# Optimization experiments

Measured on AMD Instinct MI355X. Metric: run time of the kernel, lower is better.

The kernel has to match this reference:

```python
import jax, jax.numpy as jnp
import numpy as np

NUM_HEADS = 16

def setup_inputs() -> dict:
    key = jax.random.key(0)
    ks = jax.random.split(key, 5)
    b, c, w, h = 2, 1024, 48, 48
    sc = 0.02
    return {
        "x": jax.random.normal(ks[0], (b, c, w, h), jnp.float32),
        "Wqkv": jax.random.normal(ks[1], (3 * c, c), jnp.float32) * sc,
        "bqkv": jax.random.normal(ks[2], (3 * c,), jnp.float32) * sc,
        "Wo": jax.random.normal(ks[3], (c, c), jnp.float32) * sc,
        "bo": jax.random.normal(ks[4], (c,), jnp.float32) * sc,
    }

def reference(x, Wqkv, bqkv, Wo, bo):
    b, c, w, h = x.shape
    n = NUM_HEADS
    hd = c // n
    s = w * h
    # [b,c,w,h] -> tokens [b, s, c]
    xs = x.transpose(0, 2, 3, 1).reshape(b, s, c)
    qkv = xs @ Wqkv.T + bqkv                       # [b, s, 3c]
    # rearrange 'b s (three n hd) -> three b n s hd'
    qkv = qkv.reshape(b, s, 3, n, hd).transpose(2, 0, 3, 1, 4)
    q, k, v = qkv[0], qkv[1], qkv[2]               # [b, n, s, hd]
    score = jnp.einsum('bnqh,bnkh->bnqk', q, k) / jnp.sqrt(jnp.float32(hd))
    # module uses a soft causal mask: subtract 10000 above the diagonal
    mask = 10000.0 * jnp.triu(jnp.ones((s, s), dtype=score.dtype), k=1)
    attn = jax.nn.softmax(score - mask, axis=-1)   # [b, n, s, s]
    z = jnp.einsum('bnqk,bnkh->bqnh', attn, v).reshape(b, s, c)
    out = z @ Wo.T + bo                            # [b, s, c]
    return out.reshape(b, w, h, c).transpose(0, 3, 1, 2)
```

## Files before the change

kernel.cpp:

```cpp
#include <hip/hip_runtime.h>

typedef __bf16 bf16;
typedef __bf16 bf16x8 __attribute__((ext_vector_type(8)));
typedef float floatx4 __attribute__((ext_vector_type(4)));

static constexpr int S = 2304;
static constexpr int C = 1024;
static constexpr int NHEAD = 16;
static constexpr int HDIM = 64;
static constexpr int BATCH = 2;

__global__ __launch_bounds__(256) void k_convert(const float* __restrict__ src,
                                                 bf16* __restrict__ dst, int n8) {
  int i = blockIdx.x * 256 + threadIdx.x;
  if (i >= n8) return;
  float4 a = *(const float4*)(src + (size_t)i * 8);
  float4 b = *(const float4*)(src + (size_t)i * 8 + 4);
  bf16x8 o;
  o[0] = (bf16)a.x; o[1] = (bf16)a.y; o[2] = (bf16)a.z; o[3] = (bf16)a.w;
  o[4] = (bf16)b.x; o[5] = (bf16)b.y; o[6] = (bf16)b.z; o[7] = (bf16)b.w;
  *(bf16x8*)(dst + (size_t)i * 8) = o;
}

__global__ __launch_bounds__(256) void k_transpose(const float* __restrict__ x,
                                                   bf16* __restrict__ xs) {
  __shared__ bf16 T[64 * 72];
  int c0 = blockIdx.x * 64, t0 = blockIdx.y * 64, b = blockIdx.z;
  int tid = threadIdx.x;
  const float* xb = x + (size_t)b * C * S;
#pragma unroll
  for (int it = 0; it < 4; ++it) {
    int idx = it * 256 + tid;
    int rc = idx >> 4, t4 = idx & 15;
    float4 v = *(const float4*)(xb + (size_t)(c0 + rc) * S + t0 + t4 * 4);
    T[(t4 * 4 + 0) * 72 + rc] = (bf16)v.x;
    T[(t4 * 4 + 1) * 72 + rc] = (bf16)v.y;
    T[(t4 * 4 + 2) * 72 + rc] = (bf16)v.z;
    T[(t4 * 4 + 3) * 72 + rc] = (bf16)v.w;
  }
  __syncthreads();
  bf16* xsb = xs + (size_t)b * S * C;
#pragma unroll
  for (int it = 0; it < 2; ++it) {
    int idx = it * 256 + tid;
    int rt = idx >> 3, c8 = idx & 7;
    bf16x8 v;
#pragma unroll
    for (int i = 0; i < 8; ++i) v[i] = T[rt * 72 + c8 * 8 + i];
    *(bf16x8*)(xsb + (size_t)(t0 + rt) * C + c0 + c8 * 8) = v;
  }
}

__device__ __forceinline__ void g2l16(const bf16* g, bf16* l) {
  __builtin_amdgcn_global_load_lds(
      (const __attribute__((address_space(1))) void*)g,
      (__attribute__((address_space(3))) void*)l, 16, 0, 0);
}

template <int EPI>
__global__ __launch_bounds__(256) void k_gemm_bt(const bf16* __restrict__ A,
                                                 const bf16* __restrict__ Bt,
                                                 const float* __restrict__ bias,
                                                 bf16* __restrict__ q,
                                                 bf16* __restrict__ k,
                                                 bf16* __restrict__ v,
                                                 float* __restrict__ outf) {
  constexpr int K = C;
  __shared__ bf16 As[128 * 32];
  __shared__ bf16 Bs[128 * 32];
  int tid = threadIdx.x;
  int w = tid >> 6, lane = tid & 63, ln = lane & 15, quad = lane >> 4;
  int m0 = blockIdx.y * 128, n0 = blockIdx.x * 128;
  int moff = (w >> 1) * 64, noff = (w & 1) * 64;
  floatx4 acc[4][4] = {};

  for (int k0 = 0; k0 < K; k0 += 32) {
    __syncthreads();
#pragma unroll
    for (int it = 0; it < 2; ++it) {
      int cb = (it * 4 + w) * 64;
      int g = cb + lane;
      int row = g >> 2, c4 = g & 3;
      g2l16(A + (size_t)(m0 + row) * K + k0 + c4 * 8, As + cb * 8);
      g2l16(Bt + (size_t)(n0 + row) * K + k0 + c4 * 8, Bs + cb * 8);
    }
    __syncthreads();
    bf16x8 af[4], bfr[4];
#pragma unroll
    for (int i = 0; i < 4; ++i) {
      af[i]  = *(const bf16x8*)(As + (moff + i * 16 + ln) * 32 + quad * 8);
      bfr[i] = *(const bf16x8*)(Bs + (noff + i * 16 + ln) * 32 + quad * 8);
    }
#pragma unroll
    for (int im = 0; im < 4; ++im)
#pragma unroll
      for (int in = 0; in < 4; ++in)
        acc[im][in] = __builtin_amdgcn_mfma_f32_16x16x32_bf16(
            af[im], bfr[in], acc[im][in], 0, 0, 0);
  }

  int bidx = (m0 >= S) ? 1 : 0;
  if (EPI == 0) {
#pragma unroll
    for (int in = 0; in < 4; ++in) {
      int j = n0 + noff + in * 16 + ln;
      float bv = bias[j];
      int three = j >> 10;
      int head = (j >> 6) & 15;
      int hdi = j & 63;
#pragma unroll
      for (int im = 0; im < 4; ++im) {
        int mbase = m0 + moff + im * 16 + quad * 4;
        int tb = mbase - bidx * S;
        if (three == 2) {
          union { ushort4 u; bf16 h[4]; } P;
#pragma unroll
          for (int r = 0; r < 4; ++r) P.h[r] = (bf16)(acc[im][in][r] + bv);
          *(ushort4*)(v + ((size_t)(bidx * NHEAD + head) * HDIM + hdi) * S + tb) = P.u;
        } else {
          bf16* dst = (three == 0 ? q : k) +
                      ((size_t)(bidx * NHEAD + head) * S + tb) * HDIM + hdi;
#pragma unroll
          for (int r = 0; r < 4; ++r) dst[(size_t)r * HDIM] = (bf16)(acc[im][in][r] + bv);
        }
      }
    }
  } else {
#pragma unroll
    for (int in = 0; in < 4; ++in) {
      int co = n0 + noff + in * 16 + ln;
      float bv = bias[co];
#pragma unroll
      for (int im = 0; im < 4; ++im) {
        int mbase = m0 + moff + im * 16 + quad * 4;
        int tb = mbase - bidx * S;
        float4 st;
        st.x = acc[im][in][0] + bv;
        st.y = acc[im][in][1] + bv;
        st.z = acc[im][in][2] + bv;
        st.w = acc[im][in][3] + bv;
        *(float4*)(outf + ((size_t)bidx * C + co) * S + tb) = st;
      }
    }
  }
}

__global__ __launch_bounds__(256) void k_attn(const bf16* __restrict__ Qg,
                                              const bf16* __restrict__ Kg,
                                              const bf16* __restrict__ Vtg,
                                              bf16* __restrict__ z) {
  __shared__ bf16 Ks[64 * 64];
  __shared__ bf16 Vs[64 * 64];
  __shared__ bf16 Pt[64 * 72];
  int p = blockIdx.x, h = blockIdx.y, b = blockIdx.z;
  int bh = b * NHEAD + h;
  int tid = threadIdx.x;
  int w = tid >> 6, lane = tid & 63, ln = lane & 15, quad = lane >> 4;

  const bf16* kb = Kg + (size_t)bh * S * HDIM;
  const bf16* vb = Vtg + (size_t)bh * HDIM * S;

#pragma unroll 1
  for (int half = 0; half < 2; ++half) {
    int qi = half == 0 ? p : 35 - p;
    int q0 = qi * 64;
    int qg = q0 + w * 16 + ln;

    const bf16* qb = Qg + ((size_t)bh * S + qg) * HDIM + quad * 8;
    bf16x8 qf0 = *(const bf16x8*)qb;
    bf16x8 qf1 = *(const bf16x8*)(qb + 32);

    float lsum = 0.f;
    floatx4 o_acc[4] = {};

    for (int kt = 0; kt <= qi; ++kt) {
      __syncthreads();
#pragma unroll
      for (int it = 0; it < 2; ++it) {
        int chunk = it * 256 + tid;
        int row = chunk >> 3, c8 = chunk & 7;
        int cs = c8 ^ (row & 7);
        g2l16(kb + (size_t)(kt * 64 + row) * HDIM + cs * 8, Ks + chunk * 8);
        g2l16(vb + (size_t)row * S + kt * 64 + cs * 8, Vs + chunk * 8);
      }
      __syncthreads();

      floatx4 s_acc[4] = {};
#pragma unroll
      for (int kf = 0; kf < 4; ++kf) {
        int row = kf * 16 + ln;
        int sw = row & 7;
        bf16x8 k0 = *(const bf16x8*)(Ks + row * 64 + ((0 ^ sw) ^ quad) * 8);
        s_acc[kf] = __builtin_amdgcn_mfma_f32_16x16x32_bf16(k0, qf0, s_acc[kf], 0, 0, 0);
        bf16x8 k1 = *(const bf16x8*)(Ks + row * 64 + ((4 ^ sw) ^ quad) * 8);
        s_acc[kf] = __builtin_amdgcn_mfma_f32_16x16x32_bf16(k1, qf1, s_acc[kf], 0, 0, 0);
      }

#pragma unroll
      for (int kf = 0; kf < 4; ++kf) {
        union { ushort4 u; bf16 hh[4]; } P;
#pragma unroll
        for (int r = 0; r < 4; ++r) {
          int kg = kt * 64 + kf * 16 + quad * 4 + r;
          float pv = (kg > qg) ? 0.f : exp2f(s_acc[kf][r] * 0.180336880f);
          lsum += pv;
          P.hh[r] = (bf16)pv;
        }
        *(ushort4*)(Pt + (w * 16 + ln) * 72 + kf * 16 + quad * 4) = P.u;
      }

#pragma unroll
      for (int t = 0; t < 2; ++t) {
        bf16x8 pf = *(const bf16x8*)(Pt + (w * 16 + ln) * 72 + t * 32 + quad * 8);
#pragma unroll
        for (int hf = 0; hf < 4; ++hf) {
          int row = hf * 16 + ln;
          int sw = row & 7;
          bf16x8 vf = *(const bf16x8*)(Vs + row * 64 + (((t * 4 + quad) ^ sw)) * 8);
          o_acc[hf] = __builtin_amdgcn_mfma_f32_16x16x32_bf16(vf, pf, o_acc[hf], 0, 0, 0);
        }
      }
    }

    lsum += __shfl_xor(lsum, 16);
    lsum += __shfl_xor(lsum, 32);
    float inv = 1.f / lsum;

    bf16* dst = z + ((size_t)b * S + qg) * C + h * HDIM + quad * 4;
#pragma unroll
    for (int hf = 0; hf < 4; ++hf) {
      union { ushort4 u; bf16 hh[4]; } P;
#pragma unroll
      for (int r = 0; r < 4; ++r) P.hh[r] = (bf16)(o_acc[hf][r] * inv);
      *(ushort4*)(dst + hf * 16) = P.u;
    }
    __syncthreads();
  }
}

extern "C" void kernel_launch(void* const* d_in, const int* in_sizes, int n_in,
                              void* d_out, int out_size, void* d_ws, size_t ws_size,
                              hipStream_t stream) {
  const float* x    = (const float*)d_in[0];
  const float* Wqkv = (const float*)d_in[1];
  const float* bqkv = (const float*)d_in[2];
  const float* Wo   = (const float*)d_in[3];
  const float* bo   = (const float*)d_in[4];
  float* out = (float*)d_out;

  bf16* ws = (bf16*)d_ws;
  const size_t tok = (size_t)BATCH * S * C;
  bf16* xs   = ws;
  bf16* Qg   = ws + tok;
  bf16* Kg   = ws + 2 * tok;
  bf16* Vtg  = ws + 3 * tok;
  bf16* Wqb  = ws + 4 * tok;
  bf16* Wob  = Wqb + (size_t)3 * C * C;
  bf16* z    = xs;

  k_convert<<<(3 * C * C / 8 + 255) / 256, 256, 0, stream>>>(Wqkv, Wqb, 3 * C * C / 8);
  k_convert<<<(C * C / 8 + 255) / 256, 256, 0, stream>>>(Wo, Wob, C * C / 8);
  k_transpose<<<dim3(C / 64, S / 64, BATCH), 256, 0, stream>>>(x, xs);
  k_gemm_bt<0><<<dim3(3 * C / 128, BATCH * S / 128), 256, 0, stream>>>(
      xs, Wqb, bqkv, Qg, Kg, Vtg, nullptr);
  k_attn<<<dim3(18, NHEAD, BATCH), 256, 0, stream>>>(Qg, Kg, Vtg, z);
  k_gemm_bt<1><<<dim3(C / 128, BATCH * S / 128), 256, 0, stream>>>(
      z, Wob, bo, nullptr, nullptr, nullptr, out);
}
```

Before: 240.8 us.

## Double-buffer K/V tiles and remap attention grid for XCD locality

The attention kernel now double-buffers its K/V LDS tiles. It issues the global-to-LDS loads for the next key tile before computing on the current one, so each iteration needs one barrier instead of two. The paired-half causal load balancing is replaced by a flat 1152-block grid. Block indices map so that each head stays on one XCD (bh = xcd + 8*grp) for L2 reuse of K/V, and the longest query tiles are dispatched first. This doubles the K/V LDS footprint, which may reduce occupancy, and it relies on the hardware scheduler rather than explicit pairing to balance the causal work.

```diff
diff --git a/kernel.cpp b/kernel.cpp
--- a/kernel.cpp
+++ b/kernel.cpp
@@ -149,92 +149,105 @@
                                               const bf16* __restrict__ Kg,
                                               const bf16* __restrict__ Vtg,
                                               bf16* __restrict__ z) {
-  __shared__ bf16 Ks[64 * 64];
-  __shared__ bf16 Vs[64 * 64];
+  __shared__ bf16 Ks[2][64 * 64];
+  __shared__ bf16 Vs[2][64 * 64];
   __shared__ bf16 Pt[64 * 72];
-  int p = blockIdx.x, h = blockIdx.y, b = blockIdx.z;
-  int bh = b * NHEAD + h;
+  int i = blockIdx.x;
+  int xcd = i & 7, j = i >> 3;
+  int grp = j / 36, jq = j % 36;
+  int qi = 35 - jq;
+  int bh = xcd + 8 * grp;
+  int b = bh >> 4, h = bh & 15;
   int tid = threadIdx.x;
   int w = tid >> 6, lane = tid & 63, ln = lane & 15, quad = lane >> 4;
+  int q0 = qi * 64;
+  int qg = q0 + w * 16 + ln;
 
   const bf16* kb = Kg + (size_t)bh * S * HDIM;
   const bf16* vb = Vtg + (size_t)bh * HDIM * S;
 
+  int s_row = tid >> 3, s_c8 = tid & 7;
+  int s_cs = s_c8 ^ (s_row & 7);
+  int s_row2 = (256 + tid) >> 3;
+  int s_cs2 = s_c8 ^ (s_row2 & 7);
+
+  const bf16* qb = Qg + ((size_t)bh * S + qg) * HDIM + quad * 8;
+  bf16x8 qf0 = *(const bf16x8*)qb;
+  bf16x8 qf1 = *(const bf16x8*)(qb + 32);
+
+  float lsum = 0.f;
+  floatx4 o_acc[4] = {};
+
+  {
+    g2l16(kb + (size_t)s_row * HDIM + s_cs * 8, Ks[0] + tid * 8);
+    g2l16(vb + (size_t)s_row * S + s_cs * 8, Vs[0] + tid * 8);
+    g2l16(kb + (size_t)s_row2 * HDIM + s_cs2 * 8, Ks[0] + (256 + tid) * 8);
+    g2l16(vb + (size_t)s_row2 * S + s_cs2 * 8, Vs[0] + (256 + tid) * 8);
+  }
+
 #pragma unroll 1
-  for (int half = 0; half < 2; ++half) {
-    int qi = half == 0 ? p : 35 - p;
-    int q0 = qi * 64;
-    int qg = q0 + w * 16 + ln;
-
-    const bf16* qb = Qg + ((size_t)bh * S + qg) * HDIM + quad * 8;
-    bf16x8 qf0 = *(const bf16x8*)qb;
-    bf16x8 qf1 = *(const bf16x8*)(qb + 32);
-
-    float lsum = 0.f;
-    floatx4 o_acc[4] = {};
-
-    for (int kt = 0; kt <= qi; ++kt) {
-      __syncthreads();
-#pragma unroll
-      for (int it = 0; it < 2; ++it) {
-        int chunk = it * 256 + tid;
-        int row = chunk >> 3, c8 = chunk & 7;
-        int cs = c8 ^ (row & 7);
-        g2l16(kb + (size_t)(kt * 64 + row) * HDIM + cs * 8, Ks + chunk * 8);
-        g2l16(vb + (size_t)row * S + kt * 64 + cs * 8, Vs + chunk * 8);
-      }
-      __syncthreads();
-
-      floatx4 s_acc[4] = {};
-#pragma unroll
-      for (int kf = 0; kf < 4; ++kf) {
-        int row = kf * 16 + ln;
+  for (int kt = 0; kt <= qi; ++kt) {
+    int cur = kt & 1;
+    __syncthreads();
+
+    if (kt < qi) {
+      int nxt = 1 - cur;
+      const bf16* kbn = kb + (size_t)(kt + 1) * 64 * HDIM;
+      const bf16* vbn = vb + (size_t)(kt + 1) * 64;
+      g2l16(kbn + (size_t)s_row * HDIM + s_cs * 8, Ks[nxt] + tid * 8);
+      g2l16(vbn + (size_t)s_row * S + s_cs * 8, Vs[nxt] + tid * 8);
+      g2l16(kbn + (size_t)s_row2 * HDIM + s_cs2 * 8, Ks[nxt] + (256 + tid) * 8);
+      g2l16(vbn + (size_t)s_row2 * S + s_cs2 * 8, Vs[nxt] + (256 + tid) * 8);
+    }
+
+    floatx4 s_acc[4] = {};
+#pragma unroll
+    for (int kf = 0; kf < 4; ++kf) {
+      int row = kf * 16 + ln;
+      int sw = row & 7;
+      bf16x8 k0 = *(const bf16x8*)(Ks[cur] + row * 64 + ((0 ^ sw) ^ quad) * 8);
+      s_acc[kf] = __builtin_amdgcn_mfma_f32_16x16x32_bf16(k0, qf0, s_acc[kf], 0, 0, 0);
+      bf16x8 k1 = *(const bf16x8*)(Ks[cur] + row * 64 + ((4 ^ sw) ^ quad) * 8);
+      s_acc[kf] = __builtin_amdgcn_mfma_f32_16x16x32_bf16(k1, qf1, s_acc[kf], 0, 0, 0);
+    }
+
+#pragma unroll
+    for (int kf = 0; kf < 4; ++kf) {
+      union { ushort4 u; bf16 hh[4]; } P;
+#pragma unroll
+      for (int r = 0; r < 4; ++r) {
+        int kg = kt * 64 + kf * 16 + quad * 4 + r;
+        float pv = (kg > qg) ? 0.f : exp2f(s_acc[kf][r] * 0.180336880f);
+        lsum += pv;
+        P.hh[r] = (bf16)pv;
+      }
+      *(ushort4*)(Pt + (w * 16 + ln) * 72 + kf * 16 + quad * 4) = P.u;
+    }
+
+#pragma unroll
+    for (int t = 0; t < 2; ++t) {
+      bf16x8 pf = *(const bf16x8*)(Pt + (w * 16 + ln) * 72 + t * 32 + quad * 8);
+#pragma unroll
+      for (int hf = 0; hf < 4; ++hf) {
+        int row = hf * 16 + ln;
         int sw = row & 7;
-        bf16x8 k0 = *(const bf16x8*)(Ks + row * 64 + ((0 ^ sw) ^ quad) * 8);
-        s_acc[kf] = __builtin_amdgcn_mfma_f32_16x16x32_bf16(k0, qf0, s_acc[kf], 0, 0, 0);
-        bf16x8 k1 = *(const bf16x8*)(Ks + row * 64 + ((4 ^ sw) ^ quad) * 8);
-        s_acc[kf] = __builtin_amdgcn_mfma_f32_16x16x32_bf16(k1, qf1, s_acc[kf], 0, 0, 0);
-      }
-
-#pragma unroll
-      for (int kf = 0; kf < 4; ++kf) {
-        union { ushort4 u; bf16 hh[4]; } P;
-#pragma unroll
-        for (int r = 0; r < 4; ++r) {
-          int kg = kt * 64 + kf * 16 + quad * 4 + r;
-          float pv = (kg > qg) ? 0.f : exp2f(s_acc[kf][r] * 0.180336880f);
-          lsum += pv;
-          P.hh[r] = (bf16)pv;
-        }
-        *(ushort4*)(Pt + (w * 16 + ln) * 72 + kf * 16 + quad * 4) = P.u;
-      }
-
-#pragma unroll
-      for (int t = 0; t < 2; ++t) {
-        bf16x8 pf = *(const bf16x8*)(Pt + (w * 16 + ln) * 72 + t * 32 + quad * 8);
-#pragma unroll
-        for (int hf = 0; hf < 4; ++hf) {
-          int row = hf * 16 + ln;
-          int sw = row & 7;
-          bf16x8 vf = *(const bf16x8*)(Vs + row * 64 + (((t * 4 + quad) ^ sw)) * 8);
-          o_acc[hf] = __builtin_amdgcn_mfma_f32_16x16x32_bf16(vf, pf, o_acc[hf], 0, 0, 0);
-        }
-      }
-    }
-
-    lsum += __shfl_xor(lsum, 16);
-    lsum += __shfl_xor(lsum, 32);
-    float inv = 1.f / lsum;
-
-    bf16* dst = z + ((size_t)b * S + qg) * C + h * HDIM + quad * 4;
-#pragma unroll
-    for (int hf = 0; hf < 4; ++hf) {
-      union { ushort4 u; bf16 hh[4]; } P;
-#pragma unroll
-      for (int r = 0; r < 4; ++r) P.hh[r] = (bf16)(o_acc[hf][r] * inv);
-      *(ushort4*)(dst + hf * 16) = P.u;
-    }
-    __syncthreads();
+        bf16x8 vf = *(const bf16x8*)(Vs[cur] + row * 64 + (((t * 4 + quad) ^ sw)) * 8);
+        o_acc[hf] = __builtin_amdgcn_mfma_f32_16x16x32_bf16(vf, pf, o_acc[hf], 0, 0, 0);
+      }
+    }
+  }
+
+  lsum += __shfl_xor(lsum, 16);
+  lsum += __shfl_xor(lsum, 32);
+  float inv = 1.f / lsum;
+
+  bf16* dst = z + ((size_t)b * S + qg) * C + h * HDIM + quad * 4;
+#pragma unroll
+  for (int hf = 0; hf < 4; ++hf) {
+    union { ushort4 u; bf16 hh[4]; } P;
+#pragma unroll
+    for (int r = 0; r < 4; ++r) P.hh[r] = (bf16)(o_acc[hf][r] * inv);
+    *(ushort4*)(dst + hf * 16) = P.u;
   }
 }
 
@@ -263,7 +276,7 @@
   k_transpose<<<dim3(C / 64, S / 64, BATCH), 256, 0, stream>>>(x, xs);
   k_gemm_bt<0><<<dim3(3 * C / 128, BATCH * S / 128), 256, 0, stream>>>(
       xs, Wqb, bqkv, Qg, Kg, Vtg, nullptr);
-  k_attn<<<dim3(18, NHEAD, BATCH), 256, 0, stream>>>(Qg, Kg, Vtg, z);
+  k_attn<<<dim3(1152), 256, 0, stream>>>(Qg, Kg, Vtg, z);
   k_gemm_bt<1><<<dim3(C / 128, BATCH * S / 128), 256, 0, stream>>>(
       z, Wob, bo, nullptr, nullptr, nullptr, out);
 }
```

Result: faster. 230.7 us (-4.2%).
